# Performance work log

Measured on AMD Instinct MI355X. Metric: run time of the kernel, lower is better.

## Reference

```python
import jax, jax.numpy as jnp
import numpy as np

B, S, D, H = 4, 2048, 1024, 16
DK = D // H

def setup_inputs() -> dict:
    key = jax.random.key(0)
    ks = jax.random.split(key, 8)
    scale = 1.0 / np.sqrt(D)
    q = jax.random.normal(ks[0], (B, S, D), dtype=jnp.float32)
    k = jax.random.normal(ks[1], (B, S, D), dtype=jnp.float32)
    v = jax.random.normal(ks[2], (B, S, D), dtype=jnp.float32)
    # Linear weights stored as [in, out] (applied as x @ W)
    W_q = jax.random.normal(ks[3], (D, D), dtype=jnp.float32) * scale
    W_k = jax.random.normal(ks[4], (D, D), dtype=jnp.float32) * scale
    W_v = jax.random.normal(ks[5], (D, D), dtype=jnp.float32) * scale
    W_o = jax.random.normal(ks[6], (D, D), dtype=jnp.float32) * scale
    mask = jnp.tril(jnp.ones((S, S), dtype=bool))[None, None]  # [1,1,S,S] causal
    return {"q": q, "k": k, "v": v, "W_q": W_q, "W_k": W_k, "W_v": W_v, "W_o": W_o, "mask": mask}

def reference(q, k, v, W_q, W_k, W_v, W_o, mask) -> jnp.ndarray:
    b, sq, _ = q.shape
    sk = k.shape[1]
    # project and split heads: [B,S,D] -> [B,H,S,dk]
    Q = (q @ W_q).reshape(b, sq, H, DK).transpose(0, 2, 1, 3)
    K = (k @ W_k).reshape(b, sk, H, DK).transpose(0, 2, 1, 3)
    V = (v @ W_v).reshape(b, sk, H, DK).transpose(0, 2, 1, 3)
    scores = jnp.einsum('bhqd,bhkd->bhqk', Q, K) / jnp.sqrt(jnp.float32(DK))
    scores = jnp.where(mask, scores, jnp.float32(-1e9))
    attn = jax.nn.softmax(scores, axis=-1)
    out = jnp.einsum('bhqk,bhkd->bhqd', attn, V)  # [B,H,Sq,dk]
    out = out.transpose(0, 2, 1, 3).reshape(b, sq, D)
    return out @ W_o
```

## Files before the change

### kernel.cpp

```cpp
#include <hip/hip_runtime.h>
#include <hip/hip_bf16.h>
#include <stdint.h>

#define B_  4
#define S_  2048
#define D_  1024
#define H_  16
#define DK_ 64
#define M_  (B_*S_)
#define MD_ ((size_t)M_*D_)

typedef unsigned short u16;
typedef unsigned int   u32;
using bh8 = __attribute__((ext_vector_type(8))) short;
using fx4 = __attribute__((ext_vector_type(4))) float;
using us4 = __attribute__((ext_vector_type(4))) unsigned short;

#define C1_ 0.18033688011112042f

__device__ __forceinline__ u16 f2bf(float f){
  union { float f; u32 u; } v; v.f = f;
  u32 r = v.u + 0x7FFFu + ((v.u >> 16) & 1u);
  return (u16)(r >> 16);
}
__device__ __forceinline__ u16 f2bf_fast(float f){
  union { float f; u32 u; } v; v.f = f;
  return (u16)((v.u + 0x8000u) >> 16);
}
__device__ __forceinline__ float fexp2(float x){
  float r;
  asm("v_exp_f32 %0, %1\n\ts_nop 0" : "=v"(r) : "v"(x));
  return r;
}
__device__ __forceinline__ void gl16(const void* g, void* l){
  __builtin_amdgcn_global_load_lds(
      (const __attribute__((address_space(1))) unsigned int*)g,
      (__attribute__((address_space(3))) unsigned int*)l, 16, 0, 0);
}

__global__ __launch_bounds__(256) void prep_k(const float* __restrict__ q,
                                              const float* __restrict__ k,
                                              const float* __restrict__ v,
                                              const float* __restrict__ W0,
                                              const float* __restrict__ W1,
                                              const float* __restrict__ W2,
                                              const float* __restrict__ W3,
                                              u16* __restrict__ dq,
                                              u16* __restrict__ dk,
                                              u16* __restrict__ dv,
                                              u16* __restrict__ WT){
  int id = blockIdx.x;
  int tid = threadIdx.x;
  if (id < 12288){
    int z = id >> 12;
    int i = (id & 4095)*256 + tid;
    const float* in = (z==0)? q : (z==1)? k : v;
    u16* out = (z==0)? dq : (z==1)? dk : dv;
    const float4* p = (const float4*)(in + (size_t)i*8);
    float4 a0 = p[0], a1 = p[1];
    u16 o[8];
    o[0]=f2bf(a0.x); o[1]=f2bf(a0.y); o[2]=f2bf(a0.z); o[3]=f2bf(a0.w);
    o[4]=f2bf(a1.x); o[5]=f2bf(a1.y); o[6]=f2bf(a1.z); o[7]=f2bf(a1.w);
    *(bh8*)(out + (size_t)i*8) = *(bh8*)o;
  } else {
    int id2 = id - 12288;
    int z = id2 >> 10, b2 = id2 & 1023;
    int bx = b2 & 31, by = b2 >> 5;
    const float* in = (z==0)? W0 : (z==1)? W1 : (z==2)? W2 : W3;
    float scale = (z==0)? C1_ : 1.0f;
    u16* o = WT + (size_t)z*1024*1024;
    __shared__ u16 tile[32][33];
    int tx = tid & 31, ty = tid >> 5;
    int x0 = bx*32, y0 = by*32;
    #pragma unroll
    for (int j=0;j<32;j+=8) tile[ty+j][tx] = f2bf(in[(size_t)(y0+ty+j)*D_ + x0+tx]*scale);
    __syncthreads();
    #pragma unroll
    for (int j=0;j<32;j+=8) o[(size_t)(x0+ty+j)*D_ + y0+tx] = tile[tx][ty+j];
  }
}

template<int MODE>
__global__ __launch_bounds__(256) void gemm_bt(const u16* __restrict__ Abase,
                                               const u16* __restrict__ BTbase,
                                               void* __restrict__ Cbase){
  __shared__ __align__(16) u16 Asl[2][128*64];
  __shared__ __align__(16) u16 Bsl[2][128*64];
  int z = blockIdx.z;
  const u16* A  = Abase  + (size_t)z*MD_;
  const u16* BT = BTbase + (size_t)z*1024*1024;
  int tid  = threadIdx.x;
  int w    = tid >> 6, lane = tid & 63, quad = lane >> 4, ln = lane & 15;
  int waveM = w >> 1, waveN = w & 1;
  int rowBase = blockIdx.y*128, colBase = blockIdx.x*128;

  fx4 acc[4][4];
  #pragma unroll
  for (int i=0;i<4;i++)
    #pragma unroll
    for (int j=0;j<4;j++) acc[i][j] = (fx4){0.f,0.f,0.f,0.f};

  auto stage = [&](int k0, int bi){
    #pragma unroll
    for (int i=0;i<4;i++){
      int slot = i*256 + tid;
      int kc = slot >> 7, r = slot & 127;
      gl16(&A [(size_t)(rowBase + r)*D_ + k0 + kc*8], &Asl[bi][slot*8]);
      gl16(&BT[(size_t)(colBase + r)*D_ + k0 + kc*8], &Bsl[bi][slot*8]);
    }
  };

  stage(0, 0);
  __syncthreads();

  for (int t = 0; t < 16; ++t){
    int cur = t & 1;
    if (t+1 < 16) stage((t+1)*64, cur^1);
    #pragma unroll
    for (int ks=0; ks<2; ks++){
      bh8 af[4], bf[4];
      #pragma unroll
      for (int tt=0;tt<4;tt++){
        af[tt] = *(const bh8*)(&Asl[cur][((ks*4+quad)*128 + waveM*64 + tt*16 + ln)*8]);
        bf[tt] = *(const bh8*)(&Bsl[cur][((ks*4+quad)*128 + waveN*64 + tt*16 + ln)*8]);
      }
      #pragma unroll
      for (int i=0;i<4;i++)
        #pragma unroll
        for (int j=0;j<4;j++)
          acc[i][j] = __builtin_amdgcn_mfma_f32_16x16x32_bf16(af[i], bf[j], acc[i][j], 0, 0, 0);
    }
    __syncthreads();
  }

  #pragma unroll
  for (int i=0;i<4;i++){
    int row0 = rowBase + waveM*64 + i*16 + quad*4;
    #pragma unroll
    for (int j=0;j<4;j++){
      int col = colBase + waveN*64 + j*16 + ln;
      #pragma unroll
      for (int r=0;r<4;r++){
        if (MODE == 1) ((float*)Cbase)[(size_t)(row0 + r)*D_ + col] = acc[i][j][r];
        else ((u16*)Cbase + (size_t)z*MD_)[(size_t)(row0 + r)*D_ + col] = f2bf(acc[i][j][r]);
      }
    }
  }
}

__global__ __launch_bounds__(512, 2) void gemm_qkv8(const u16* __restrict__ Aqk,
                                                    const u16* __restrict__ Av,
                                                    const u16* __restrict__ WTb,
                                                    u16* __restrict__ Cqk,
                                                    u16* __restrict__ VtOut){
  __shared__ __align__(16) u16 AL[2][2][8192];
  __shared__ __align__(16) u16 BL[2][2][8192];
  int z = blockIdx.z;
  const u16* A  = (z < 2) ? (Aqk + (size_t)z*MD_) : Av;
  const u16* BT = WTb + (size_t)z*1024*1024;
  int tid = threadIdx.x;
  int w = tid >> 6, lane = tid & 63, quad = lane >> 4, ln = lane & 15;
  int wm = w >> 2, wn = w & 3;
  int rowBase = blockIdx.y*256, colBase = blockIdx.x*256;

  auto stageHT = [&](int mat, int kt, int hf){
    int buf = kt & 1;
    u16* dst = mat ? &BL[buf][hf][0] : &AL[buf][hf][0];
    const u16* src = mat ? BT : A;
    int gbase = (mat ? colBase : rowBase) + hf*128;
    int k0 = kt*64;
    #pragma unroll
    for (int j=0;j<2;j++){
      int slot = j*512 + tid;
      int kc = slot >> 7, r = slot & 127;
      gl16(&src[(size_t)(gbase + r)*D_ + k0 + kc*8], dst + slot*8);
    }
  };

  fx4 acc[8][4];
  #pragma unroll
  for (int i=0;i<8;i++)
    #pragma unroll
    for (int j=0;j<4;j++) acc[i][j] = (fx4){0.f,0.f,0.f,0.f};

  stageHT(0,0,0); stageHT(0,0,1);
  stageHT(1,0,0); stageHT(1,0,1);
  stageHT(1,1,0); stageHT(1,1,1);
  asm volatile("s_waitcnt vmcnt(4)" ::: "memory");
  __builtin_amdgcn_s_barrier();

  bh8 bfr[4][2];
  for (int it = 0; it < 8; ++it){
    int t = 2*it;
    #pragma unroll
    for (int p = 0; p < 8; ++p){
      const int buf = p >> 2;
      const int q = p & 3;
      const u16* Ah = &AL[buf][wm][0];
      const u16* Bh = &BL[buf][wn>>1][0];

      if (q == 0){
        #pragma unroll
        for (int n=0;n<4;n++)
          #pragma unroll
          for (int ks=0;ks<2;ks++)
            bfr[n][ks] = *(const bh8*)(&Bh[((ks*4+quad)*128 + (wn&1)*64 + n*16 + ln)*8]);
      }
      bh8 af[2][2];
      #pragma unroll
      for (int mi=0;mi<2;mi++)
        #pragma unroll
        for (int ks=0;ks<2;ks++)
          af[mi][ks] = *(const bh8*)(&Ah[((ks*4+quad)*128 + (q*2+mi)*16 + ln)*8]);

      switch(p){
        case 0: stageHT(0, t+1, 0); break;
        case 1: stageHT(0, t+1, 1); break;
        case 2: if (t+2 < 16) stageHT(1, t+2, 0); break;
        case 3: if (t+2 < 16) stageHT(1, t+2, 1); break;
        case 4: if (t+2 < 16) stageHT(0, t+2, 0); break;
        case 5: if (t+2 < 16) stageHT(0, t+2, 1); break;
        case 6: if (t+3 < 16) stageHT(1, t+3, 0); break;
        case 7: if (t+3 < 16) stageHT(1, t+3, 1); break;
      }

      if (p == 3){
        if (t+2 < 16) asm volatile("s_waitcnt vmcnt(4)" ::: "memory");
        else          asm volatile("s_waitcnt vmcnt(0)" ::: "memory");
      }
      if (p == 7 && t+2 < 16) asm volatile("s_waitcnt vmcnt(4)" ::: "memory");

      __builtin_amdgcn_s_barrier();
      asm volatile("s_waitcnt lgkmcnt(0)" ::: "memory");

      __builtin_amdgcn_s_setprio(1);
      #pragma unroll
      for (int mi=0;mi<2;mi++)
        #pragma unroll
        for (int n=0;n<4;n++)
          #pragma unroll
          for (int ks=0;ks<2;ks++)
            acc[q*2+mi][n] = __builtin_amdgcn_mfma_f32_16x16x32_bf16(
                                af[mi][ks], bfr[n][ks], acc[q*2+mi][n], 0,0,0);
      __builtin_amdgcn_s_setprio(0);
      __builtin_amdgcn_s_barrier();
    }
  }

  #pragma unroll
  for (int m=0;m<8;m++){
    int row0 = rowBase + wm*128 + m*16 + quad*4;
    #pragma unroll
    for (int n=0;n<4;n++){
      int col = colBase + wn*64 + n*16 + ln;
      if (z == 2){
        int bb = row0 >> 11, tok = row0 & (S_-1);
        int hh = col >> 6,  vd  = col & 63;
        us4 pk;
        #pragma unroll
        for (int r=0;r<4;r++) pk[r] = f2bf(acc[m][n][r]);
        *(us4*)&VtOut[((size_t)((bb*16+hh)*64+vd))*S_ + tok] = pk;
      } else {
        #pragma unroll
        for (int r=0;r<4;r++)
          (Cqk + (size_t)z*MD_)[(size_t)(row0 + r)*D_ + col] = f2bf(acc[m][n][r]);
      }
    }
  }
}

__global__ __launch_bounds__(256) void attn_k(const u16* __restrict__ Q,
                                              const u16* __restrict__ Kp,
                                              const u16* __restrict__ VtG,
                                              u16* __restrict__ O){
  __shared__ __align__(16) u16 Kt[2][64*64];
  __shared__ __align__(16) u16 Vt[2][64*64];
  __shared__ __align__(16) u16 Pb[4*16*64];

  int bh = blockIdx.x; int b = bh>>4, h = bh&15;
  int qt = (int)gridDim.y - 1 - (int)blockIdx.y;
  int tid = threadIdx.x;
  int w = tid >> 6, lane = tid & 63, quad = lane >> 4, ln = lane & 15;
  int q0w = qt*128 + w*32;
  size_t headoff = (size_t)h*DK_;

  bh8 qf[2][2];
  #pragma unroll
  for (int rg=0; rg<2; rg++){
    const u16* qp = Q + (size_t)(b*S_ + q0w + rg*16 + ln)*D_ + headoff + quad*8;
    qf[rg][0] = *(const bh8*)qp;
    qf[rg][1] = *(const bh8*)(qp + 32);
  }

  float m_i[2], l_i[2];
  fx4 oacc[2][4];
  #pragma unroll
  for (int rg=0; rg<2; rg++){
    m_i[rg] = -3e38f; l_i[rg] = 0.f;
    #pragma unroll
    for (int r=0;r<4;r++) oacc[rg][r] = (fx4){0.f,0.f,0.f,0.f};
  }

  auto stage = [&](int k0, int bi){
    #pragma unroll
    for (int i=0;i<2;i++){
      int s = i*256 + tid;
      int n = s >> 3, kc = (s & 7) ^ (n & 7);
      gl16(&Kp[(size_t)(b*S_ + k0 + n)*D_ + headoff + kc*8], &Kt[bi][s*8]);
    }
    #pragma unroll
    for (int i=0;i<2;i++){
      int s = i*256 + tid;
      int vd = s >> 3, c = (s & 7) ^ (vd & 7);
      gl16(&VtG[(size_t)(bh*64 + vd)*S_ + k0 + c*8], &Vt[bi][s*8]);
    }
  };

  u16* Pw = &Pb[w*16*64];
  int ntiles = 2*qt + 2;

  stage(0, 0);
  __syncthreads();

  for (int kt=0; kt<ntiles; kt++){
    int cur = kt & 1;
    if (kt+1 < ntiles) stage((kt+1)*64, cur^1);
    const u16* Kc = Kt[cur];
    const u16* Vc = Vt[cur];
    int k0 = kt*64;
    bool diag = (kt >= 2*qt);

    #pragma unroll
    for (int rg=0; rg<2; rg++){
      fx4 sacc[4];
      #pragma unroll
      for (int t=0;t<4;t++){
        int n = t*16 + ln;
        bh8 kf0 = *(const bh8*)(&Kc[(n*8 + ( quad    ^ (ln&7)))*8]);
        bh8 kf1 = *(const bh8*)(&Kc[(n*8 + ((4+quad) ^ (ln&7)))*8]);
        fx4 zz = (fx4){0.f,0.f,0.f,0.f};
        zz = __builtin_amdgcn_mfma_f32_16x16x32_bf16(kf0, qf[rg][0], zz, 0,0,0);
        zz = __builtin_amdgcn_mfma_f32_16x16x32_bf16(kf1, qf[rg][1], zz, 0,0,0);
        sacc[t] = zz;
      }

      int qg = q0w + rg*16 + ln;
      if (diag){
        #pragma unroll
        for (int t=0;t<4;t++){
          #pragma unroll
          for (int r=0;r<4;r++){
            int kg = k0 + t*16 + quad*4 + r;
            sacc[t][r] = (kg <= qg) ? sacc[t][r] : -3e38f;
          }
        }
      }

      float tm[4];
      #pragma unroll
      for (int t=0;t<4;t++)
        tm[t] = fmaxf(fmaxf(sacc[t][0], sacc[t][1]), fmaxf(sacc[t][2], sacc[t][3]));
      float mloc = fmaxf(fmaxf(tm[0], tm[1]), fmaxf(tm[2], tm[3]));
      mloc = fmaxf(mloc, __shfl_xor(mloc, 16, 64));
      mloc = fmaxf(mloc, __shfl_xor(mloc, 32, 64));

      float mn = fmaxf(m_i[rg], mloc);
      float alpha = fexp2(m_i[rg] - mn);
      m_i[rg] = mn;

      float ts[4];
      #pragma unroll
      for (int t=0;t<4;t++){
        #pragma unroll
        for (int r=0;r<4;r++) sacc[t][r] = fexp2(sacc[t][r] - mn);
        ts[t] = (sacc[t][0] + sacc[t][1]) + (sacc[t][2] + sacc[t][3]);
      }
      float rs = (ts[0] + ts[1]) + (ts[2] + ts[3]);
      rs += __shfl_xor(rs, 16, 64);
      rs += __shfl_xor(rs, 32, 64);
      l_i[rg] = l_i[rg]*alpha + rs;

      float al[4];
      #pragma unroll
      for (int r=0;r<4;r++) al[r] = __shfl(alpha, quad*4 + r, 64);
      #pragma unroll
      for (int vt=0;vt<4;vt++)
        #pragma unroll
        for (int r=0;r<4;r++)
          oacc[rg][vt][r] *= al[r];

      #pragma unroll
      for (int t=0;t<4;t++){
        int c = 2*t + (quad>>1);
        us4 pk;
        #pragma unroll
        for (int r=0;r<4;r++) pk[r] = f2bf_fast(sacc[t][r]);
        *(us4*)&Pw[(ln*8 + (c ^ (ln&7)))*8 + (quad&1)*4] = pk;
      }
      asm volatile("s_waitcnt lgkmcnt(0)" ::: "memory");

      __builtin_amdgcn_s_setprio(1);
      #pragma unroll
      for (int s2=0; s2<2; s2++){
        int c = s2*4 + quad;
        bh8 pf = *(const bh8*)(&Pw[(ln*8 + (c ^ (ln&7)))*8]);
        #pragma unroll
        for (int vt=0; vt<4; vt++){
          int vd = vt*16 + ln;
          bh8 vf = *(const bh8*)(&Vc[(vd*8 + (c ^ (ln&7)))*8]);
          oacc[rg][vt] = __builtin_amdgcn_mfma_f32_16x16x32_bf16(pf, vf, oacc[rg][vt], 0,0,0);
        }
      }
      __builtin_amdgcn_s_setprio(0);
      asm volatile("s_waitcnt lgkmcnt(0)" ::: "memory");
    }
    __syncthreads();
  }

  #pragma unroll
  for (int rg=0; rg<2; rg++){
    float linv = 1.0f / l_i[rg];
    float lb[4];
    #pragma unroll
    for (int r=0;r<4;r++) lb[r] = __shfl(linv, quad*4 + r, 64);
    #pragma unroll
    for (int r=0;r<4;r++){
      #pragma unroll
      for (int vt=0; vt<4; vt++){
        float ov = oacc[rg][vt][r] * lb[r];
        O[(size_t)(b*S_ + q0w + rg*16 + quad*4 + r)*D_ + headoff + vt*16 + ln] = f2bf(ov);
      }
    }
  }
}

extern "C" void kernel_launch(void* const* d_in, const int* in_sizes, int n_in,
                              void* d_out, int out_size, void* d_ws, size_t ws_size,
                              hipStream_t stream){
  const float* q  = (const float*)d_in[0];
  const float* k  = (const float*)d_in[1];
  const float* v  = (const float*)d_in[2];
  const float* Wq = (const float*)d_in[3];
  const float* Wk = (const float*)d_in[4];
  const float* Wv = (const float*)d_in[5];
  const float* Wo = (const float*)d_in[6];

  u16* ws  = (u16*)d_ws;
  u16* WT  = ws;
  u16* xa  = WT + (size_t)4*1024*1024;
  u16* xb  = xa + MD_;
  u16* Qp  = xb + MD_;
  u16* Kp  = Qp + MD_;

  u16* vb  = (u16*)d_out;
  u16* VtG = vb + MD_;

  prep_k<<<dim3(16384), 256, 0, stream>>>(q, k, v, Wq, Wk, Wv, Wo, xa, xb, vb, WT);

  gemm_qkv8<<<dim3(4,32,3), 512, 0, stream>>>(xa, vb, WT, Qp, VtG);

  attn_k<<<dim3(B_*H_, S_/128), 256, 0, stream>>>(Qp, Kp, VtG, Qp);

  gemm_bt<1><<<dim3(8,64,1), 256, 0, stream>>>(Qp, WT + (size_t)3*1024*1024, d_out);
}
```

Measured before the change: 374.6 us.

## Unify projection GEMMs into swizzled 128x256 tile kernel with XCD-aware block mapping

Replaces the separate QKV and output-projection GEMM kernels with one templated 512-thread kernel. It uses 128x256 tiles, an XOR-swizzled LDS layout to avoid bank conflicts, a reworked double-buffered prefetch schedule, and a 1D grid remapped so neighbouring tiles land on the same XCD for L2 reuse. The output projection now uses the same pipelined kernel instead of the simpler 256-thread one. The change trades larger per-block tiles for more blocks and better cache locality, at the risk of different occupancy and a more fragile wait-count schedule.

Measured after the change: 327.0 us. 12.7% less time.

```diff
diff --git a/kernel.cpp b/kernel.cpp
--- a/kernel.cpp
+++ b/kernel.cpp
@@ -81,158 +81,107 @@
 }
 
 template<int MODE>
-__global__ __launch_bounds__(256) void gemm_bt(const u16* __restrict__ Abase,
-                                               const u16* __restrict__ BTbase,
-                                               void* __restrict__ Cbase){
-  __shared__ __align__(16) u16 Asl[2][128*64];
-  __shared__ __align__(16) u16 Bsl[2][128*64];
-  int z = blockIdx.z;
-  const u16* A  = Abase  + (size_t)z*MD_;
-  const u16* BT = BTbase + (size_t)z*1024*1024;
-  int tid  = threadIdx.x;
-  int w    = tid >> 6, lane = tid & 63, quad = lane >> 4, ln = lane & 15;
-  int waveM = w >> 1, waveN = w & 1;
-  int rowBase = blockIdx.y*128, colBase = blockIdx.x*128;
-
-  fx4 acc[4][4];
-  #pragma unroll
-  for (int i=0;i<4;i++)
-    #pragma unroll
-    for (int j=0;j<4;j++) acc[i][j] = (fx4){0.f,0.f,0.f,0.f};
-
-  auto stage = [&](int k0, int bi){
-    #pragma unroll
-    for (int i=0;i<4;i++){
-      int slot = i*256 + tid;
-      int kc = slot >> 7, r = slot & 127;
-      gl16(&A [(size_t)(rowBase + r)*D_ + k0 + kc*8], &Asl[bi][slot*8]);
-      gl16(&BT[(size_t)(colBase + r)*D_ + k0 + kc*8], &Bsl[bi][slot*8]);
-    }
-  };
-
-  stage(0, 0);
-  __syncthreads();
-
-  for (int t = 0; t < 16; ++t){
-    int cur = t & 1;
-    if (t+1 < 16) stage((t+1)*64, cur^1);
-    #pragma unroll
-    for (int ks=0; ks<2; ks++){
-      bh8 af[4], bf[4];
-      #pragma unroll
-      for (int tt=0;tt<4;tt++){
-        af[tt] = *(const bh8*)(&Asl[cur][((ks*4+quad)*128 + waveM*64 + tt*16 + ln)*8]);
-        bf[tt] = *(const bh8*)(&Bsl[cur][((ks*4+quad)*128 + waveN*64 + tt*16 + ln)*8]);
-      }
-      #pragma unroll
-      for (int i=0;i<4;i++)
-        #pragma unroll
-        for (int j=0;j<4;j++)
-          acc[i][j] = __builtin_amdgcn_mfma_f32_16x16x32_bf16(af[i], bf[j], acc[i][j], 0, 0, 0);
-    }
-    __syncthreads();
-  }
-
-  #pragma unroll
-  for (int i=0;i<4;i++){
-    int row0 = rowBase + waveM*64 + i*16 + quad*4;
-    #pragma unroll
-    for (int j=0;j<4;j++){
-      int col = colBase + waveN*64 + j*16 + ln;
-      #pragma unroll
-      for (int r=0;r<4;r++){
-        if (MODE == 1) ((float*)Cbase)[(size_t)(row0 + r)*D_ + col] = acc[i][j][r];
-        else ((u16*)Cbase + (size_t)z*MD_)[(size_t)(row0 + r)*D_ + col] = f2bf(acc[i][j][r]);
-      }
-    }
-  }
-}
-
-__global__ __launch_bounds__(512, 2) void gemm_qkv8(const u16* __restrict__ Aqk,
-                                                    const u16* __restrict__ Av,
-                                                    const u16* __restrict__ WTb,
-                                                    u16* __restrict__ Cqk,
-                                                    u16* __restrict__ VtOut){
-  __shared__ __align__(16) u16 AL[2][2][8192];
-  __shared__ __align__(16) u16 BL[2][2][8192];
-  int z = blockIdx.z;
-  const u16* A  = (z < 2) ? (Aqk + (size_t)z*MD_) : Av;
+__global__ __launch_bounds__(512) void gemm8(const u16* __restrict__ Aqk,
+                                             const u16* __restrict__ Av,
+                                             const u16* __restrict__ WTb,
+                                             u16* __restrict__ Cqk,
+                                             u16* __restrict__ VtOut,
+                                             float* __restrict__ Cf){
+  __shared__ __align__(16) u16 AL[2][128*64];
+  __shared__ __align__(16) u16 BL[2][256*64];
+
+  int hbid = blockIdx.x;
+  int xcd = hbid & 7, slot = hbid >> 3;
+  int pg  = xcd * (MODE==0 ? 24 : 8) + (slot >> 2);
+  int x   = slot & 3;
+  int y   = (MODE==0) ? (pg & 63) : pg;
+  int z   = (MODE==0) ? (pg >> 6) : 0;
+
+  const u16* A  = (MODE==0 && z==2) ? Av : (Aqk + (size_t)z*MD_);
   const u16* BT = WTb + (size_t)z*1024*1024;
   int tid = threadIdx.x;
   int w = tid >> 6, lane = tid & 63, quad = lane >> 4, ln = lane & 15;
   int wm = w >> 2, wn = w & 3;
-  int rowBase = blockIdx.y*256, colBase = blockIdx.x*256;
-
-  auto stageHT = [&](int mat, int kt, int hf){
-    int buf = kt & 1;
-    u16* dst = mat ? &BL[buf][hf][0] : &AL[buf][hf][0];
-    const u16* src = mat ? BT : A;
-    int gbase = (mat ? colBase : rowBase) + hf*128;
-    int k0 = kt*64;
-    #pragma unroll
-    for (int j=0;j<2;j++){
-      int slot = j*512 + tid;
-      int kc = slot >> 7, r = slot & 127;
-      gl16(&src[(size_t)(gbase + r)*D_ + k0 + kc*8], dst + slot*8);
-    }
+  int rowBase = y*128, colBase = x*256;
+
+  auto sA = [&](int buf, int kt, int c){
+    int s = c*512 + tid;
+    int row = s >> 3, kc = (s & 7) ^ (row & 7);
+    gl16(&A[(size_t)(rowBase + row)*D_ + kt*64 + kc*8], &AL[buf][s*8]);
   };
-
-  fx4 acc[8][4];
+  auto sB = [&](int buf, int kt, int c){
+    int s = c*512 + tid;
+    int row = s >> 3, kc = (s & 7) ^ (row & 7);
+    gl16(&BT[(size_t)(colBase + row)*D_ + kt*64 + kc*8], &BL[buf][s*8]);
+  };
+  auto ridx = [&](int row, int kc){ return row*64 + ((kc ^ (row & 7))*8); };
+
+  fx4 acc[4][4];
   #pragma unroll
-  for (int i=0;i<8;i++)
+  for (int i=0;i<4;i++)
     #pragma unroll
     for (int j=0;j<4;j++) acc[i][j] = (fx4){0.f,0.f,0.f,0.f};
 
-  stageHT(0,0,0); stageHT(0,0,1);
-  stageHT(1,0,0); stageHT(1,0,1);
-  stageHT(1,1,0); stageHT(1,1,1);
-  asm volatile("s_waitcnt vmcnt(4)" ::: "memory");
+  sA(0,0,0); sA(0,0,1); sB(0,0,0); sB(0,0,1); sB(0,0,2); sB(0,0,3);
+  sB(1,1,0); sB(1,1,1); sB(1,1,2);
+  asm volatile("s_waitcnt vmcnt(3)" ::: "memory");
   __builtin_amdgcn_s_barrier();
 
-  bh8 bfr[4][2];
   for (int it = 0; it < 8; ++it){
     int t = 2*it;
-    #pragma unroll
-    for (int p = 0; p < 8; ++p){
-      const int buf = p >> 2;
-      const int q = p & 3;
-      const u16* Ah = &AL[buf][wm][0];
-      const u16* Bh = &BL[buf][wn>>1][0];
-
-      if (q == 0){
+    bool h2 = (t+2 < 16), h3 = (t+3 < 16);
+    #pragma unroll
+    for (int half = 0; half < 2; ++half){
+      const u16* Ab = &AL[half][0];
+      const u16* Bb = &BL[half][0];
+
+      bh8 bfr[4][2], af0[2][2], af1[2][2];
+      #pragma unroll
+      for (int n=0;n<4;n++)
+        #pragma unroll
+        for (int ks=0;ks<2;ks++)
+          bfr[n][ks] = *(const bh8*)(&Bb[ridx(wn*64 + n*16 + ln, ks*4+quad)]);
+      #pragma unroll
+      for (int mi=0;mi<2;mi++)
+        #pragma unroll
+        for (int ks=0;ks<2;ks++)
+          af0[mi][ks] = *(const bh8*)(&Ab[ridx(wm*64 + mi*16 + ln, ks*4+quad)]);
+      #pragma unroll
+      for (int mi=0;mi<2;mi++)
+        #pragma unroll
+        for (int ks=0;ks<2;ks++)
+          af1[mi][ks] = *(const bh8*)(&Ab[ridx(wm*64 + 32 + mi*16 + ln, ks*4+quad)]);
+
+      if (half == 0){
+        sB(1, t+1, 3); sA(1, t+1, 0); sA(1, t+1, 1);
+      } else if (h2){
+        sB(0, t+2, 3); sA(0, t+2, 0); sA(0, t+2, 1);
+      }
+      __builtin_amdgcn_s_barrier();
+      asm volatile("s_waitcnt lgkmcnt(4)" ::: "memory");
+      __builtin_amdgcn_s_setprio(1);
+      #pragma unroll
+      for (int mi=0;mi<2;mi++)
         #pragma unroll
         for (int n=0;n<4;n++)
           #pragma unroll
           for (int ks=0;ks<2;ks++)
-            bfr[n][ks] = *(const bh8*)(&Bh[((ks*4+quad)*128 + (wn&1)*64 + n*16 + ln)*8]);
-      }
-      bh8 af[2][2];
-      #pragma unroll
-      for (int mi=0;mi<2;mi++)
-        #pragma unroll
-        for (int ks=0;ks<2;ks++)
-          af[mi][ks] = *(const bh8*)(&Ah[((ks*4+quad)*128 + (q*2+mi)*16 + ln)*8]);
-
-      switch(p){
-        case 0: stageHT(0, t+1, 0); break;
-        case 1: stageHT(0, t+1, 1); break;
-        case 2: if (t+2 < 16) stageHT(1, t+2, 0); break;
-        case 3: if (t+2 < 16) stageHT(1, t+2, 1); break;
-        case 4: if (t+2 < 16) stageHT(0, t+2, 0); break;
-        case 5: if (t+2 < 16) stageHT(0, t+2, 1); break;
-        case 6: if (t+3 < 16) stageHT(1, t+3, 0); break;
-        case 7: if (t+3 < 16) stageHT(1, t+3, 1); break;
-      }
-
-      if (p == 3){
-        if (t+2 < 16) asm volatile("s_waitcnt vmcnt(4)" ::: "memory");
-        else          asm volatile("s_waitcnt vmcnt(0)" ::: "memory");
-      }
-      if (p == 7 && t+2 < 16) asm volatile("s_waitcnt vmcnt(4)" ::: "memory");
-
+            acc[mi][n] = __builtin_amdgcn_mfma_f32_16x16x32_bf16(
+                            af0[mi][ks], bfr[n][ks], acc[mi][n], 0,0,0);
+      __builtin_amdgcn_s_setprio(0);
+      __builtin_amdgcn_s_barrier();
+
+      if (half == 0){
+        if (h2){ sB(0, t+2, 0); sB(0, t+2, 1); sB(0, t+2, 2); }
+        if (h2) asm volatile("s_waitcnt vmcnt(3)" ::: "memory");
+        else    asm volatile("s_waitcnt vmcnt(0)" ::: "memory");
+      } else {
+        if (h3){ sB(1, t+3, 0); sB(1, t+3, 1); sB(1, t+3, 2); }
+        if (h3) asm volatile("s_waitcnt vmcnt(3)" ::: "memory");
+        else    asm volatile("s_waitcnt vmcnt(0)" ::: "memory");
+      }
       __builtin_amdgcn_s_barrier();
       asm volatile("s_waitcnt lgkmcnt(0)" ::: "memory");
-
       __builtin_amdgcn_s_setprio(1);
       #pragma unroll
       for (int mi=0;mi<2;mi++)
@@ -240,20 +189,24 @@
         for (int n=0;n<4;n++)
           #pragma unroll
           for (int ks=0;ks<2;ks++)
-            acc[q*2+mi][n] = __builtin_amdgcn_mfma_f32_16x16x32_bf16(
-                                af[mi][ks], bfr[n][ks], acc[q*2+mi][n], 0,0,0);
+            acc[2+mi][n] = __builtin_amdgcn_mfma_f32_16x16x32_bf16(
+                              af1[mi][ks], bfr[n][ks], acc[2+mi][n], 0,0,0);
       __builtin_amdgcn_s_setprio(0);
       __builtin_amdgcn_s_barrier();
     }
   }
 
   #pragma unroll
-  for (int m=0;m<8;m++){
-    int row0 = rowBase + wm*128 + m*16 + quad*4;
+  for (int m=0;m<4;m++){
+    int row0 = rowBase + wm*64 + m*16 + quad*4;
     #pragma unroll
     for (int n=0;n<4;n++){
       int col = colBase + wn*64 + n*16 + ln;
-      if (z == 2){
+      if (MODE == 1){
+        #pragma unroll
+        for (int r=0;r<4;r++)
+          Cf[(size_t)(row0 + r)*D_ + col] = acc[m][n][r];
+      } else if (z == 2){
         int bb = row0 >> 11, tok = row0 & (S_-1);
         int hh = col >> 6,  vd  = col & 63;
         us4 pk;
@@ -457,9 +410,10 @@
 
   prep_k<<<dim3(16384), 256, 0, stream>>>(q, k, v, Wq, Wk, Wv, Wo, xa, xb, vb, WT);
 
-  gemm_qkv8<<<dim3(4,32,3), 512, 0, stream>>>(xa, vb, WT, Qp, VtG);
+  gemm8<0><<<dim3(768), 512, 0, stream>>>(xa, vb, WT, Qp, VtG, nullptr);
 
   attn_k<<<dim3(B_*H_, S_/128), 256, 0, stream>>>(Qp, Kp, VtG, Qp);
 
-  gemm_bt<1><<<dim3(8,64,1), 256, 0, stream>>>(Qp, WT + (size_t)3*1024*1024, d_out);
-}
+  gemm8<1><<<dim3(256), 512, 0, stream>>>(Qp, nullptr, WT + (size_t)3*1024*1024,
+                                          nullptr, nullptr, (float*)d_out);
+}
```
